# Optimization experiments

Hardware: AMD Instinct MI355X
Metric: run time of the kernel (lower is better)

Reference implementation:

```python
import jax, jax.numpy as jnp
import numpy as np

B, S, D = 8, 1024, 1024

def setup_inputs() -> dict:
    key = jax.random.key(0)
    ks = jax.random.split(key, 6)
    context = jax.random.normal(ks[0], (B, S, D), dtype=jnp.float32)
    eos_mask = jax.random.randint(ks[1], (B, S), 0, 2, dtype=jnp.int32)
    prior = jax.random.uniform(ks[2], (), dtype=jnp.float32)
    adj_mat = jax.random.randint(ks[3], (B, S, S), 0, 2, dtype=jnp.int32)
    Wk = jax.random.normal(ks[4], (D, D), dtype=jnp.float32) * 0.02
    Wq = jax.random.normal(ks[5], (D, D), dtype=jnp.float32) * 0.02
    bk = jnp.zeros((D,), jnp.float32)
    bq = jnp.zeros((D,), jnp.float32)
    ln_gamma = jnp.ones((D,), jnp.float32)
    ln_beta = jnp.zeros((D,), jnp.float32)
    return {"context": context, "eos_mask": eos_mask, "prior": prior,
            "adj_mat": adj_mat, "Wk": Wk, "bk": bk, "Wq": Wq, "bq": bq,
            "ln_gamma": ln_gamma, "ln_beta": ln_beta}

def reference(context, eos_mask, prior, adj_mat, Wk, bk, Wq, bq, ln_gamma, ln_beta):
    d_model = context.shape[-1]
    seq_len = context.shape[1]
    # LayerNorm (annotated-transformer style: unbiased std, eps added to std)
    mu = jnp.mean(context, axis=-1, keepdims=True)
    std = jnp.std(context, axis=-1, keepdims=True, ddof=1)
    x = ln_gamma * (context - mu) / (std + 1e-6) + ln_beta
    # projections (torch Linear: x @ W.T + b)
    key_p = x @ Wk.T + bk
    query = x @ Wq.T + bq
    scores = jnp.einsum('bqd,bkd->bqk', query, key_p) / (d_model / 2)
    scores = jnp.where(adj_mat == 0, -1e9, scores)
    neibor_attn = jax.nn.softmax(scores, axis=-1)
    neibor_attn = jnp.sqrt(neibor_attn * jnp.swapaxes(neibor_attn, -1, -2) + 1e-9)
    neibor_attn = prior + (1.0 - prior) * neibor_attn
    # constant structural matrices
    a = jnp.eye(seq_len, k=1, dtype=jnp.float32)          # superdiagonal
    b = jnp.eye(seq_len, dtype=jnp.float32)               # diagonal
    tri = jnp.triu(jnp.ones((seq_len, seq_len), jnp.float32))  # upper incl diag
    # t = (log(attn+eps) masked to superdiagonal) @ tri
    t = jnp.matmul(jnp.where(a == 0, 0.0, jnp.log(neibor_attn + 1e-9)), tri)
    g_attn = jnp.exp(jnp.matmul(tri, t))
    g_attn = jnp.where((tri - b) == 0, 0.0, g_attn)  # keep strict upper only
    g_attn = g_attn + jnp.swapaxes(g_attn, -1, -2) + jnp.where(b == 0, 1e-9, neibor_attn)
    return (g_attn, neibor_attn)
```

## Files before the change

kernel.cpp:

```cpp
#include <hip/hip_runtime.h>
#include <hip/hip_bf16.h>

#define S_LEN 1024
#define D_DIM 1024
#define N_BAT 8
#define BSS   (8ull*1024ull*1024ull)

using bf16x8 = __attribute__((ext_vector_type(8))) short;
using f32x4  = __attribute__((ext_vector_type(4))) float;

__device__ __forceinline__ short f2bf(float v) {
    __hip_bfloat16 h = __float2bfloat16(v);
    return *reinterpret_cast<short*>(&h);
}

__device__ __forceinline__ void gload_lds16(const void* g, void* l) {
    __builtin_amdgcn_global_load_lds(
        (const __attribute__((address_space(1))) void*)g,
        (__attribute__((address_space(3))) void*)l, 16, 0, 0);
}

template<int KITERS>
__device__ __forceinline__ void gemm_mainloop256(
    const short* __restrict__ A, const short* __restrict__ Bt,
    int brow, int bcol, int kstart,
    short* As, short* Bs, f32x4 acc[4][4])
{
    const int tid  = threadIdx.x;
    const int lane = tid & 63;
    const int w    = tid >> 6;
    const int wr   = w >> 1;
    const int wc   = w & 1;
    const int rsel = lane & 15;
    const int kb   = (lane >> 4) * 16;
    const int sw   = (rsel & 7) << 4;

    const int srow  = tid >> 3;
    const int scolb = ((tid & 7) * 16) ^ ((srow & 7) << 4);
    const int sdst  = tid * 16;

#pragma unroll
    for (int m = 0; m < 4; ++m)
#pragma unroll
        for (int n = 0; n < 4; ++n) acc[m][n] = 0.0f;

    auto stage = [&](int slot, int k0) {
        char* Ad = (char*)As + slot * 32768;
        char* Bd = (char*)Bs + slot * 16384;
#pragma unroll
        for (int c = 0; c < 4; ++c) {
            const int row = c * 64 + srow;
            gload_lds16((const char*)(A + (size_t)(brow + row) * 1024 + k0) + scolb,
                        Ad + c * 8192 + sdst);
        }
#pragma unroll
        for (int c = 0; c < 2; ++c) {
            const int row = c * 64 + srow;
            gload_lds16((const char*)(Bt + (size_t)(bcol + row) * 1024 + k0) + scolb,
                        Bd + c * 8192 + sdst);
        }
    };

    stage(0, kstart);
    if (KITERS > 1) stage(1, kstart + 64);

#pragma unroll
    for (int t = 0; t < KITERS; ++t) {
        if (t < KITERS - 1) asm volatile("s_waitcnt vmcnt(6)" ::: "memory");
        else                asm volatile("s_waitcnt vmcnt(0)" ::: "memory");
        __builtin_amdgcn_s_barrier();
        asm volatile("" ::: "memory");

        const char* Ac = (const char*)As + (t % 3) * 32768;
        const char* Bc = (const char*)Bs + (t % 3) * 16384;
        bf16x8 af[4][2], bfr[4][2];
#pragma unroll
        for (int m = 0; m < 4; ++m) {
            const int row = wr * 64 + m * 16 + rsel;
#pragma unroll
            for (int kk = 0; kk < 2; ++kk)
                af[m][kk] = *(const bf16x8*)&Ac[row * 128 + ((kk * 64 + kb) ^ sw)];
        }
#pragma unroll
        for (int n = 0; n < 4; ++n) {
            const int row = wc * 64 + n * 16 + rsel;
#pragma unroll
            for (int kk = 0; kk < 2; ++kk)
                bfr[n][kk] = *(const bf16x8*)&Bc[row * 128 + ((kk * 64 + kb) ^ sw)];
        }

        if (t + 2 < KITERS) stage((t + 2) % 3, kstart + (t + 2) * 64);

        __builtin_amdgcn_s_setprio(1);
#pragma unroll
        for (int kk = 0; kk < 2; ++kk)
#pragma unroll
            for (int m = 0; m < 4; ++m)
#pragma unroll
                for (int n = 0; n < 4; ++n)
                    acc[m][n] = __builtin_amdgcn_mfma_f32_16x16x32_bf16(
                        af[m][kk], bfr[n][kk], acc[m][n], 0, 0, 0);
        __builtin_amdgcn_s_setprio(0);
    }
}

__global__ __launch_bounds__(512) void gemm_bf16(
    const short* __restrict__ A, const short* __restrict__ Bt,
    short* __restrict__ C)
{
    __shared__ short As[3 * 16384];
    __shared__ short Bs[3 * 8192];
    const int flat = blockIdx.x + 32 * blockIdx.y;
    const int nid  = (flat & 7) * 32 + (flat >> 3);
    const int mx   = nid >> 3;
    const int ny   = nid & 7;
    const int brow = mx * 256, bcol = ny * 128;

    f32x4 acc[4][4];
    gemm_mainloop256<16>(A, Bt, brow, bcol, 0, As, Bs, acc);

    const int lane = threadIdx.x & 63;
    const int w    = threadIdx.x >> 6;
    const int wr   = w >> 1, wc = w & 1;
#pragma unroll
    for (int m = 0; m < 4; ++m)
#pragma unroll
        for (int n = 0; n < 4; ++n) {
            const int colg = bcol + wc * 64 + n * 16 + (lane & 15);
#pragma unroll
            for (int r = 0; r < 4; ++r) {
                const int rowg = brow + wr * 64 + m * 16 + ((lane >> 4) * 4 + r);
                C[(size_t)rowg * 1024 + colg] = f2bf(acc[m][n][r]);
            }
        }
}

__global__ __launch_bounds__(512) void gemm_scores(
    const short* __restrict__ Tm, const short* __restrict__ Xm,
    const float* __restrict__ p, const float* __restrict__ r2,
    const float* __restrict__ c0p, const int* __restrict__ adj,
    float* __restrict__ Sc)
{
    __shared__ short As[3 * 16384];
    __shared__ short Bs[3 * 8192];
    const int flat = blockIdx.x + 4 * blockIdx.y + 32 * blockIdx.z;
    const int nid  = (flat & 7) * 32 + (flat >> 3);
    const int b    = nid >> 5;
    const int rem  = nid & 31;
    const int mx   = rem & 3;
    const int ny   = rem >> 2;
    const short* A  = Tm + (size_t)b * 1024 * 1024;
    const short* Bt = Xm + (size_t)b * 1024 * 1024;
    const float* pb = p  + (size_t)b * 1024;
    const float* rb = r2 + (size_t)b * 1024;
    const int*   ab = adj + (size_t)b * 1024 * 1024;
    float* C = Sc + (size_t)b * 1024 * 1024;
    const int brow = mx * 256, bcol = ny * 128;

    f32x4 acc[4][4];
    gemm_mainloop256<16>(A, Bt, brow, bcol, 0, As, Bs, acc);

    const int lane = threadIdx.x & 63;
    const int w    = threadIdx.x >> 6;
    const int wr   = w >> 1, wc = w & 1;
    const float c0v = c0p[0];
#pragma unroll
    for (int m = 0; m < 4; ++m)
#pragma unroll
        for (int n = 0; n < 4; ++n) {
            const int colg = bcol + wc * 64 + n * 16 + (lane & 15);
            const float radd = rb[colg] + c0v;
#pragma unroll
            for (int r = 0; r < 4; ++r) {
                const int rowg = brow + wr * 64 + m * 16 + ((lane >> 4) * 4 + r);
                const size_t idx = (size_t)rowg * 1024 + colg;
                const float val = (acc[m][n][r] + pb[rowg] + radd) * 0.001953125f;
                C[idx] = ab[idx] ? val : -1e9f;
            }
        }
}

__global__ __launch_bounds__(512) void gemm_splitk(
    const short* __restrict__ A, const short* __restrict__ Bt,
    float* __restrict__ P)
{
    __shared__ short As[3 * 16384];
    __shared__ short Bs[3 * 8192];
    const int brow = blockIdx.x * 256, bcol = blockIdx.y * 128;
    const int z = blockIdx.z;

    f32x4 acc[4][4];
    gemm_mainloop256<4>(A, Bt, brow, bcol, z * 256, As, Bs, acc);

    float* Pz = P + (size_t)z * 1024 * 1024;
    const int lane = threadIdx.x & 63;
    const int w    = threadIdx.x >> 6;
    const int wr   = w >> 1, wc = w & 1;
#pragma unroll
    for (int m = 0; m < 4; ++m)
#pragma unroll
        for (int n = 0; n < 4; ++n) {
            const int colg = bcol + wc * 64 + n * 16 + (lane & 15);
#pragma unroll
            for (int r = 0; r < 4; ++r) {
                const int rowg = brow + wr * 64 + m * 16 + ((lane >> 4) * 4 + r);
                Pz[(size_t)rowg * 1024 + colg] = acc[m][n][r];
            }
        }
}

__global__ __launch_bounds__(256) void reduce_m2t(
    const float* __restrict__ P, short* __restrict__ M)
{
    const int idx = blockIdx.x * 256 + threadIdx.x;
    const float4* P4 = (const float4*)P;
    float4 s = P4[idx];
    const float4 s1 = P4[idx + 262144];
    const float4 s2 = P4[idx + 524288];
    const float4 s3 = P4[idx + 786432];
    s.x += s1.x + s2.x + s3.x;
    s.y += s1.y + s2.y + s3.y;
    s.z += s1.z + s2.z + s3.z;
    s.w += s1.w + s2.w + s3.w;
    short4 o;
    o.x = f2bf(s.x); o.y = f2bf(s.y); o.z = f2bf(s.z); o.w = f2bf(s.w);
    ((short4*)M)[idx] = o;
}

__global__ __launch_bounds__(256) void bias_gemv1(
    const float* __restrict__ Wq, const float* __restrict__ Wk,
    const float* __restrict__ bk, const float* __restrict__ bq,
    float* __restrict__ pu, float* __restrict__ pv)
{
    __shared__ float su[8][128];
    __shared__ float sv[8][128];
    const int tx = threadIdx.x & 31;
    const int ty = threadIdx.x >> 5;
    const int colBase = blockIdx.x * 128;
    const int rowBase = blockIdx.y * 64;
    const int i = colBase + tx * 4;
    float4 au = {0,0,0,0}, av = {0,0,0,0};
#pragma unroll
    for (int jj = 0; jj < 8; ++jj) {
        const int j = rowBase + ty + jj * 8;
        const float bkv = bk[j], bqv = bq[j];
        const float4 wq = *(const float4*)&Wq[(size_t)j * 1024 + i];
        const float4 wk = *(const float4*)&Wk[(size_t)j * 1024 + i];
        au.x += wq.x * bkv; au.y += wq.y * bkv; au.z += wq.z * bkv; au.w += wq.w * bkv;
        av.x += wk.x * bqv; av.y += wk.y * bqv; av.z += wk.z * bqv; av.w += wk.w * bqv;
    }
    ((float4*)su[ty])[tx] = au;
    ((float4*)sv[ty])[tx] = av;
    __syncthreads();
    if (ty == 0) {
        float4 s1 = ((float4*)su[0])[tx];
        float4 s2 = ((float4*)sv[0])[tx];
#pragma unroll
        for (int k = 1; k < 8; ++k) {
            const float4 t1 = ((float4*)su[k])[tx];
            const float4 t2 = ((float4*)sv[k])[tx];
            s1.x += t1.x; s1.y += t1.y; s1.z += t1.z; s1.w += t1.w;
            s2.x += t2.x; s2.y += t2.y; s2.z += t2.z; s2.w += t2.w;
        }
        ((float4*)&pu[(size_t)blockIdx.y * 1024 + colBase])[tx] = s1;
        ((float4*)&pv[(size_t)blockIdx.y * 1024 + colBase])[tx] = s2;
    }
}

__global__ __launch_bounds__(256) void bias_gemv2(
    const float* __restrict__ pu, const float* __restrict__ pv,
    const float* __restrict__ bk, const float* __restrict__ bq,
    float* __restrict__ u, float* __restrict__ v, float* __restrict__ c0)
{
    __shared__ float sh[4];
    const int i = blockIdx.x * 256 + threadIdx.x;
    float su = 0.0f, sv = 0.0f;
#pragma unroll
    for (int k = 0; k < 16; ++k) {
        su += pu[k * 1024 + i];
        sv += pv[k * 1024 + i];
    }
    u[i] = su;
    v[i] = sv;
    if (blockIdx.x == 0) {
        const int t = threadIdx.x;
        const float4 a = ((const float4*)bq)[t];
        const float4 b = ((const float4*)bk)[t];
        float s = a.x*b.x + a.y*b.y + a.z*b.z + a.w*b.w;
        for (int off = 32; off > 0; off >>= 1) s += __shfl_down(s, off);
        const int lane = t & 63, w = t >> 6;
        if (lane == 0) sh[w] = s;
        __syncthreads();
        if (t == 0) c0[0] = sh[0] + sh[1] + sh[2] + sh[3];
    }
}

__global__ __launch_bounds__(256) void ln_kernel(
    const float* __restrict__ X, const float* __restrict__ gamma,
    const float* __restrict__ beta, const float* __restrict__ u,
    const float* __restrict__ v2, short* __restrict__ Y,
    float* __restrict__ p, float* __restrict__ r2)
{
    __shared__ float sh[16];
    const size_t row = blockIdx.x;
    const int t = threadIdx.x;
    float4 v = ((const float4*)(X + row * 1024))[t];
    float s  = v.x + v.y + v.z + v.w;
    float ss = v.x*v.x + v.y*v.y + v.z*v.z + v.w*v.w;
    for (int off = 32; off > 0; off >>= 1) {
        s  += __shfl_down(s, off);
        ss += __shfl_down(ss, off);
    }
    const int lane = t & 63, w = t >> 6;
    if (lane == 0) { sh[w] = s; sh[4 + w] = ss; }
    __syncthreads();
    if (t == 0) {
        float S  = sh[0] + sh[1] + sh[2] + sh[3];
        float SS = sh[4] + sh[5] + sh[6] + sh[7];
        float mu = S * (1.0f / 1024.0f);
        float var = fmaxf((SS - S * mu) * (1.0f / 1023.0f), 0.0f);
        sh[0] = mu;
        sh[1] = 1.0f / (sqrtf(var) + 1e-6f);
    }
    __syncthreads();
    const float mu = sh[0], inv = sh[1];
    float4 g  = ((const float4*)gamma)[t];
    float4 be = ((const float4*)beta)[t];
    float y0 = g.x * (v.x - mu) * inv + be.x;
    float y1 = g.y * (v.y - mu) * inv + be.y;
    float y2 = g.z * (v.z - mu) * inv + be.z;
    float y3 = g.w * (v.w - mu) * inv + be.w;
    short4 o;
    o.x = f2bf(y0); o.y = f2bf(y1); o.z = f2bf(y2); o.w = f2bf(y3);
    ((short4*)(Y + row * 1024))[t] = o;
    float4 uu = ((const float4*)u)[t];
    float4 vv = ((const float4*)v2)[t];
    float dp = y0*uu.x + y1*uu.y + y2*uu.z + y3*uu.w;
    float dr = y0*vv.x + y1*vv.y + y2*vv.z + y3*vv.w;
    for (int off = 32; off > 0; off >>= 1) {
        dp += __shfl_down(dp, off);
        dr += __shfl_down(dr, off);
    }
    if (lane == 0) { sh[8 + w] = dp; sh[12 + w] = dr; }
    __syncthreads();
    if (t == 0) {
        p[row]  = sh[8] + sh[9] + sh[10] + sh[11];
        r2[row] = sh[12] + sh[13] + sh[14] + sh[15];
    }
}

__global__ __launch_bounds__(256) void cvt_t_kernel(
    const float* __restrict__ Wq, const float* __restrict__ Wk,
    short* __restrict__ wqt, short* __restrict__ wkt)
{
    __shared__ float T[32][33];
    const float* src = blockIdx.z ? Wk : Wq;
    short* dst = blockIdx.z ? wkt : wqt;
    const int bi = blockIdx.x * 32, bj = blockIdx.y * 32;
    const int c = threadIdx.x & 31, r0 = threadIdx.x >> 5;
#pragma unroll
    for (int rr = 0; rr < 4; ++rr) {
        const int r = r0 + rr * 8;
        T[r][c] = src[(size_t)(bi + r) * 1024 + bj + c];
    }
    __syncthreads();
#pragma unroll
    for (int rr = 0; rr < 4; ++rr) {
        const int r = r0 + rr * 8;
        dst[(size_t)(bj + r) * 1024 + bi + c] = f2bf(T[c][r]);
    }
}

__global__ __launch_bounds__(256) void rowstat_kernel(
    const float* __restrict__ Sc, float2* __restrict__ stats)
{
    __shared__ float sh[4];
    const size_t row = blockIdx.x;
    const int t = threadIdx.x;
    const float4 sv = ((const float4*)(Sc + row * 1024))[t];
    float m = fmaxf(fmaxf(sv.x, sv.y), fmaxf(sv.z, sv.w));
    for (int off = 32; off > 0; off >>= 1) m = fmaxf(m, __shfl_down(m, off));
    const int lane = t & 63, w = t >> 6;
    if (lane == 0) sh[w] = m;
    __syncthreads();
    const float M = fmaxf(fmaxf(sh[0], sh[1]), fmaxf(sh[2], sh[3]));
    __syncthreads();
    float s = expf(sv.x - M) + expf(sv.y - M) + expf(sv.z - M) + expf(sv.w - M);
    for (int off = 32; off > 0; off >>= 1) s += __shfl_down(s, off);
    if (lane == 0) sh[w] = s;
    __syncthreads();
    if (t == 0) {
        const float Sm = sh[0] + sh[1] + sh[2] + sh[3];
        stats[row] = make_float2(M, 1.0f / Sm);
    }
}

__global__ __launch_bounds__(1024) void cum2_kernel(
    const float* __restrict__ Sc, const float2* __restrict__ stats,
    const float* __restrict__ prior_p, double* __restrict__ cum)
{
    __shared__ double sh[1024];
    const int b = blockIdx.x;
    const int t = threadIdx.x;
    const float prior = *prior_p;
    const float om = 1.0f - prior;
    const float* sc = Sc + (size_t)b * 1024 * 1024;
    const float2* st = stats + (size_t)b * 1024;
    double v = 0.0;
    if (t >= 1) {
        const int k = t - 1;
        const float2 s1 = st[k], s2 = st[k + 1];
        const float a1 = expf(sc[(size_t)k * 1024 + (k + 1)] - s1.x) * s1.y;
        const float a2 = expf(sc[(size_t)(k + 1) * 1024 + k] - s2.x) * s2.y;
        const float na = prior + om * sqrtf(a1 * a2 + 1e-9f);
        v = (double)logf(na + 1e-9f);
    }
    sh[t] = v;
    __syncthreads();
#pragma unroll
    for (int off = 1; off < 1024; off <<= 1) {
        const double add = (t >= off) ? sh[t - off] : 0.0;
        __syncthreads();
        sh[t] += add;
        __syncthreads();
    }
    cum[b * 1024 + t] = sh[t];
}

__global__ __launch_bounds__(256) void na_g2_kernel(
    float* __restrict__ Sc, const float2* __restrict__ stats,
    const float* __restrict__ prior_p, const double* __restrict__ cum,
    float* __restrict__ NA)
{
    const int flat = blockIdx.x + 1024 * blockIdx.y;
    const int nid  = (flat & 7) * 1024 + (flat >> 3);
    const int b    = nid >> 10;
    const int tidx = nid & 1023;
    const int ti = tidx >> 5, tj = tidx & 31;
    if (tj < ti) return;
    const float prior = *prior_p;
    const float om = 1.0f - prior;
    float* sc = Sc + (size_t)b * 1024 * 1024;
    float* na = NA + (size_t)b * 1024 * 1024;
    const float2* st = stats + (size_t)b * 1024;
    const double* cb = cum + (size_t)b * 1024;
    __shared__ float T1[32][33];
    __shared__ float T2[32][33];
    const int c = threadIdx.x & 31, r0 = threadIdx.x >> 5;
#pragma unroll
    for (int rr = 0; rr < 4; ++rr) {
        const int r = r0 + rr * 8;
        const int R1 = ti * 32 + r, R2 = tj * 32 + r;
        const float2 s1 = st[R1], s2 = st[R2];
        T1[r][c] = expf(sc[(size_t)R1 * 1024 + tj * 32 + c] - s1.x) * s1.y;
        T2[r][c] = expf(sc[(size_t)R2 * 1024 + ti * 32 + c] - s2.x) * s2.y;
    }
    __syncthreads();
#pragma unroll
    for (int rr = 0; rr < 4; ++rr) {
        const int r = r0 + rr * 8;
        const int R1 = ti * 32 + r, C1 = tj * 32 + c;
        const float na1 = prior + om * sqrtf(T1[r][c] * T2[c][r] + 1e-9f);
        na[(size_t)R1 * 1024 + C1] = na1;
        float g1;
        if (R1 == C1) g1 = na1;
        else {
            const int lo = min(R1, C1), hi = max(R1, C1);
            g1 = expf((float)(cb[hi] - cb[lo])) + 1e-9f;
        }
        sc[(size_t)R1 * 1024 + C1] = g1;
        const int R2 = tj * 32 + r, C2 = ti * 32 + c;
        const float na2 = prior + om * sqrtf(T2[r][c] * T1[c][r] + 1e-9f);
        na[(size_t)R2 * 1024 + C2] = na2;
        float g2;
        if (R2 == C2) g2 = na2;
        else {
            const int lo = min(R2, C2), hi = max(R2, C2);
            g2 = expf((float)(cb[hi] - cb[lo])) + 1e-9f;
        }
        sc[(size_t)R2 * 1024 + C2] = g2;
    }
}

extern "C" void kernel_launch(void* const* d_in, const int* in_sizes, int n_in,
                              void* d_out, int out_size, void* d_ws, size_t ws_size,
                              hipStream_t stream)
{
    const float* context = (const float*)d_in[0];
    const float* prior   = (const float*)d_in[2];
    const int*   adj     = (const int*)d_in[3];
    const float* Wk      = (const float*)d_in[4];
    const float* bk      = (const float*)d_in[5];
    const float* Wq      = (const float*)d_in[6];
    const float* bq      = (const float*)d_in[7];
    const float* gamma   = (const float*)d_in[8];
    const float* beta    = (const float*)d_in[9];

    float* out   = (float*)d_out;
    float* gout  = out;
    float* naout = out + BSS;

    char* ws = (char*)d_ws;
    short*  xb    = (short*)(ws);
    short*  wqt   = (short*)(ws + (16ull << 20));
    short*  wkt   = (short*)(ws + (18ull << 20));
    short*  m2t   = (short*)(ws + (20ull << 20));
    short*  tb    = (short*)(ws + (22ull << 20));
    float*  m2par = (float*)tb;
    double* cumd  = (double*)(ws + (38ull << 20));
    float*  uvec  = (float*)(ws + (38ull << 20) + (1ull << 16));
    float*  vvec  = uvec + 1024;
    float*  c0    = vvec + 1024;
    float*  pvec  = c0 + 64;
    float*  rvec  = pvec + 8192;
    float*  pu    = rvec + 8192;
    float*  pv    = pu + 16384;
    float2* statv = (float2*)(pv + 16384);

    bias_gemv1<<<dim3(8, 16), 256, 0, stream>>>(Wq, Wk, bk, bq, pu, pv);
    bias_gemv2<<<4, 256, 0, stream>>>(pu, pv, bk, bq, uvec, vvec, c0);
    ln_kernel<<<8192, 256, 0, stream>>>(context, gamma, beta, uvec, vvec,
                                        xb, pvec, rvec);
    cvt_t_kernel<<<dim3(32, 32, 2), 256, 0, stream>>>(Wq, Wk, wqt, wkt);
    gemm_splitk<<<dim3(4, 8, 4), 512, 0, stream>>>(wkt, wqt, m2par);
    reduce_m2t<<<1024, 256, 0, stream>>>(m2par, m2t);
    gemm_bf16<<<dim3(32, 8), 512, 0, stream>>>(xb, m2t, tb);
    gemm_scores<<<dim3(4, 8, 8), 512, 0, stream>>>(tb, xb, pvec, rvec, c0,
                                                   adj, gout);
    rowstat_kernel<<<8192, 256, 0, stream>>>(gout, statv);
    cum2_kernel<<<8, 1024, 0, stream>>>(gout, statv, prior, cumd);
    na_g2_kernel<<<dim3(1024, 8), 256, 0, stream>>>(gout, statv, prior, cumd,
                                                    naout);
}
```

Measured before the change: 123.2 us.

## Switch GEMMs to 256x256 tiles with 8-phase double-buffered pipelined mainloop

Replaces the 256x128 triple-buffered GEMM mainloop with a 256x256 tile, double-buffered, 4-phase-per-k-tile schedule. Global-to-LDS loads for the next tile are interleaved between MFMA quadrants, and barriers separate the phases. Each wave now computes 128x64 outputs with 8x4 accumulators, which raises reuse per LDS read. Grids are halved to match the larger tiles. The risks are fewer blocks (128 per GEMM on a large GPU), which can underfill CUs, and higher register pressure from the 32 accumulators.

```diff
diff --git a/kernel.cpp b/kernel.cpp
--- a/kernel.cpp
+++ b/kernel.cpp
@@ -20,133 +20,169 @@
         (__attribute__((address_space(3))) void*)l, 16, 0, 0);
 }
 
-template<int KITERS>
-__device__ __forceinline__ void gemm_mainloop256(
+#define RD_A(dst, bufb, MH)                                                  \
+    {                                                                        \
+        const char* _b = (const char*)As + (bufb);                           \
+        _Pragma("unroll")                                                    \
+        for (int _m = 0; _m < 4; ++_m) {                                     \
+            const int _row = wr * 128 + ((MH) * 4 + _m) * 16 + rsel;         \
+            const int _sw  = (_row & 7) << 4;                                \
+            _Pragma("unroll")                                                \
+            for (int _kk = 0; _kk < 2; ++_kk)                                \
+                dst[_m * 2 + _kk] = *(const bf16x8*)&_b[_row * 128 +         \
+                                        ((_kk * 64 + kb) ^ _sw)];            \
+        }                                                                    \
+    }
+
+#define RD_B(dst, bufb, NH)                                                  \
+    {                                                                        \
+        const char* _b = (const char*)Bs + (bufb);                           \
+        _Pragma("unroll")                                                    \
+        for (int _n = 0; _n < 2; ++_n) {                                     \
+            const int _row = wc * 64 + ((NH) * 2 + _n) * 16 + rsel;          \
+            const int _sw  = (_row & 7) << 4;                                \
+            _Pragma("unroll")                                                \
+            for (int _kk = 0; _kk < 2; ++_kk)                                \
+                dst[_n * 2 + _kk] = *(const bf16x8*)&_b[_row * 128 +         \
+                                        ((_kk * 64 + kb) ^ _sw)];            \
+        }                                                                    \
+    }
+
+#define MMA_Q(av, bv, MH, NH)                                                \
+    __builtin_amdgcn_s_setprio(1);                                           \
+    _Pragma("unroll")                                                        \
+    for (int _kk = 0; _kk < 2; ++_kk)                                        \
+        _Pragma("unroll")                                                    \
+        for (int _m = 0; _m < 4; ++_m)                                       \
+            _Pragma("unroll")                                                \
+            for (int _n = 0; _n < 2; ++_n)                                   \
+                acc[(MH) * 4 + _m][(NH) * 2 + _n] =                          \
+                    __builtin_amdgcn_mfma_f32_16x16x32_bf16(                 \
+                        av[_m * 2 + _kk], bv[_n * 2 + _kk],                  \
+                        acc[(MH) * 4 + _m][(NH) * 2 + _n], 0, 0, 0);         \
+    __builtin_amdgcn_s_setprio(0);
+
+#define PHASE_END()                                                          \
+    __builtin_amdgcn_s_barrier();                                            \
+    __builtin_amdgcn_sched_barrier(0);
+
+template<int KTILES>
+__device__ __forceinline__ void gemm_ml_8ph(
     const short* __restrict__ A, const short* __restrict__ Bt,
     int brow, int bcol, int kstart,
-    short* As, short* Bs, f32x4 acc[4][4])
+    short* As, short* Bs, f32x4 acc[8][4])
 {
     const int tid  = threadIdx.x;
     const int lane = tid & 63;
     const int w    = tid >> 6;
-    const int wr   = w >> 1;
-    const int wc   = w & 1;
+    const int wr   = w >> 2;
+    const int wc   = w & 3;
     const int rsel = lane & 15;
     const int kb   = (lane >> 4) * 16;
-    const int sw   = (rsel & 7) << 4;
-
-    const int srow  = tid >> 3;
-    const int scolb = ((tid & 7) * 16) ^ ((srow & 7) << 4);
-    const int sdst  = tid * 16;
-
-#pragma unroll
-    for (int m = 0; m < 4; ++m)
+
+    const int f0 = tid;
+    const int f1 = 512 + tid;
+    const int r0 = f0 >> 3, cb0 = ((f0 & 7) * 16) ^ ((r0 & 7) << 4);
+    const int r1 = f1 >> 3, cb1 = ((f1 & 7) * 16) ^ ((r1 & 7) << 4);
+
+#pragma unroll
+    for (int m = 0; m < 8; ++m)
 #pragma unroll
         for (int n = 0; n < 4; ++n) acc[m][n] = 0.0f;
 
-    auto stage = [&](int slot, int k0) {
-        char* Ad = (char*)As + slot * 32768;
-        char* Bd = (char*)Bs + slot * 16384;
-#pragma unroll
-        for (int c = 0; c < 4; ++c) {
-            const int row = c * 64 + srow;
-            gload_lds16((const char*)(A + (size_t)(brow + row) * 1024 + k0) + scolb,
-                        Ad + c * 8192 + sdst);
-        }
-#pragma unroll
-        for (int c = 0; c < 2; ++c) {
-            const int row = c * 64 + srow;
-            gload_lds16((const char*)(Bt + (size_t)(bcol + row) * 1024 + k0) + scolb,
-                        Bd + c * 8192 + sdst);
-        }
+    auto stageA = [&](int buf, int h, int k0) {
+        char* d = (char*)As + buf * 32768 + h * 16384;
+        gload_lds16((const char*)(A + (size_t)(brow + h * 128 + r0) * 1024 + k0) + cb0,
+                    d + f0 * 16);
+        gload_lds16((const char*)(A + (size_t)(brow + h * 128 + r1) * 1024 + k0) + cb1,
+                    d + f1 * 16);
     };
-
-    stage(0, kstart);
-    if (KITERS > 1) stage(1, kstart + 64);
-
-#pragma unroll
-    for (int t = 0; t < KITERS; ++t) {
-        if (t < KITERS - 1) asm volatile("s_waitcnt vmcnt(6)" ::: "memory");
-        else                asm volatile("s_waitcnt vmcnt(0)" ::: "memory");
+    auto stageB = [&](int buf, int h, int k0) {
+        char* d = (char*)Bs + buf * 32768 + h * 16384;
+        gload_lds16((const char*)(Bt + (size_t)(bcol + h * 128 + r0) * 1024 + k0) + cb0,
+                    d + f0 * 16);
+        gload_lds16((const char*)(Bt + (size_t)(bcol + h * 128 + r1) * 1024 + k0) + cb1,
+                    d + f1 * 16);
+    };
+
+    stageA(0, 0, kstart); stageA(0, 1, kstart);
+    stageB(0, 0, kstart); stageB(0, 1, kstart);
+
+    bf16x8 a[8], b0[4], b1[4];
+    for (int t = 0; t < KTILES; ++t) {
+        const int cur = t & 1, nxt = cur ^ 1;
+        const int curb = cur * 32768;
+        const int kn = kstart + (t + 1) * 64;
+        const bool pre = (t + 1 < KTILES);
+        if (pre) {
+            stageA(nxt, 0, kn);
+            asm volatile("s_waitcnt vmcnt(2)" ::: "memory");
+        } else {
+            asm volatile("s_waitcnt vmcnt(0)" ::: "memory");
+        }
         __builtin_amdgcn_s_barrier();
-        asm volatile("" ::: "memory");
-
-        const char* Ac = (const char*)As + (t % 3) * 32768;
-        const char* Bc = (const char*)Bs + (t % 3) * 16384;
-        bf16x8 af[4][2], bfr[4][2];
-#pragma unroll
-        for (int m = 0; m < 4; ++m) {
-            const int row = wr * 64 + m * 16 + rsel;
-#pragma unroll
-            for (int kk = 0; kk < 2; ++kk)
-                af[m][kk] = *(const bf16x8*)&Ac[row * 128 + ((kk * 64 + kb) ^ sw)];
-        }
-#pragma unroll
-        for (int n = 0; n < 4; ++n) {
-            const int row = wc * 64 + n * 16 + rsel;
-#pragma unroll
-            for (int kk = 0; kk < 2; ++kk)
-                bfr[n][kk] = *(const bf16x8*)&Bc[row * 128 + ((kk * 64 + kb) ^ sw)];
-        }
-
-        if (t + 2 < KITERS) stage((t + 2) % 3, kstart + (t + 2) * 64);
-
-        __builtin_amdgcn_s_setprio(1);
-#pragma unroll
-        for (int kk = 0; kk < 2; ++kk)
-#pragma unroll
-            for (int m = 0; m < 4; ++m)
-#pragma unroll
-                for (int n = 0; n < 4; ++n)
-                    acc[m][n] = __builtin_amdgcn_mfma_f32_16x16x32_bf16(
-                        af[m][kk], bfr[n][kk], acc[m][n], 0, 0, 0);
-        __builtin_amdgcn_s_setprio(0);
-    }
-}
-
-__global__ __launch_bounds__(512) void gemm_bf16(
+        __builtin_amdgcn_sched_barrier(0);
+        RD_A(a, curb, 0);
+        RD_B(b0, curb, 0);
+        MMA_Q(a, b0, 0, 0);
+        PHASE_END();
+        if (pre) stageA(nxt, 1, kn);
+        RD_B(b1, curb, 1);
+        MMA_Q(a, b1, 0, 1);
+        PHASE_END();
+        if (pre) stageB(nxt, 0, kn);
+        RD_A(a, curb, 1);
+        MMA_Q(a, b1, 1, 1);
+        PHASE_END();
+        if (pre) stageB(nxt, 1, kn);
+        MMA_Q(a, b0, 1, 0);
+        PHASE_END();
+    }
+}
+
+__global__ __launch_bounds__(512, 2) void gemm_bf16(
     const short* __restrict__ A, const short* __restrict__ Bt,
     short* __restrict__ C)
 {
-    __shared__ short As[3 * 16384];
-    __shared__ short Bs[3 * 8192];
+    __shared__ short As[2 * 16384];
+    __shared__ short Bs[2 * 16384];
     const int flat = blockIdx.x + 32 * blockIdx.y;
-    const int nid  = (flat & 7) * 32 + (flat >> 3);
-    const int mx   = nid >> 3;
-    const int ny   = nid & 7;
-    const int brow = mx * 256, bcol = ny * 128;
-
-    f32x4 acc[4][4];
-    gemm_mainloop256<16>(A, Bt, brow, bcol, 0, As, Bs, acc);
+    const int nid  = (flat & 7) * 16 + (flat >> 3);
+    const int mx   = nid >> 2;
+    const int ny   = nid & 3;
+    const int brow = mx * 256, bcol = ny * 256;
+
+    f32x4 acc[8][4];
+    gemm_ml_8ph<16>(A, Bt, brow, bcol, 0, As, Bs, acc);
 
     const int lane = threadIdx.x & 63;
     const int w    = threadIdx.x >> 6;
-    const int wr   = w >> 1, wc = w & 1;
-#pragma unroll
-    for (int m = 0; m < 4; ++m)
-#pragma unroll
-        for (int n = 0; n < 4; ++n) {
-            const int colg = bcol + wc * 64 + n * 16 + (lane & 15);
+    const int wr   = w >> 2, wc = w & 3;
+#pragma unroll
+    for (int mm = 0; mm < 8; ++mm)
+#pragma unroll
+        for (int nn = 0; nn < 4; ++nn) {
+            const int colg = bcol + wc * 64 + nn * 16 + (lane & 15);
 #pragma unroll
             for (int r = 0; r < 4; ++r) {
-                const int rowg = brow + wr * 64 + m * 16 + ((lane >> 4) * 4 + r);
-                C[(size_t)rowg * 1024 + colg] = f2bf(acc[m][n][r]);
+                const int rowg = brow + wr * 128 + mm * 16 + ((lane >> 4) * 4 + r);
+                C[(size_t)rowg * 1024 + colg] = f2bf(acc[mm][nn][r]);
             }
         }
 }
 
-__global__ __launch_bounds__(512) void gemm_scores(
+__global__ __launch_bounds__(512, 2) void gemm_scores(
     const short* __restrict__ Tm, const short* __restrict__ Xm,
     const float* __restrict__ p, const float* __restrict__ r2,
     const float* __restrict__ c0p, const int* __restrict__ adj,
     float* __restrict__ Sc)
 {
-    __shared__ short As[3 * 16384];
-    __shared__ short Bs[3 * 8192];
-    const int flat = blockIdx.x + 4 * blockIdx.y + 32 * blockIdx.z;
-    const int nid  = (flat & 7) * 32 + (flat >> 3);
-    const int b    = nid >> 5;
-    const int rem  = nid & 31;
+    __shared__ short As[2 * 16384];
+    __shared__ short Bs[2 * 16384];
+    const int flat = blockIdx.x + 4 * blockIdx.y + 16 * blockIdx.z;
+    const int nid  = (flat & 7) * 16 + (flat >> 3);
+    const int b    = nid >> 4;
+    const int rem  = nid & 15;
     const int mx   = rem & 3;
     const int ny   = rem >> 2;
     const short* A  = Tm + (size_t)b * 1024 * 1024;
@@ -155,56 +191,56 @@
     const float* rb = r2 + (size_t)b * 1024;
     const int*   ab = adj + (size_t)b * 1024 * 1024;
     float* C = Sc + (size_t)b * 1024 * 1024;
-    const int brow = mx * 256, bcol = ny * 128;
-
-    f32x4 acc[4][4];
-    gemm_mainloop256<16>(A, Bt, brow, bcol, 0, As, Bs, acc);
+    const int brow = mx * 256, bcol = ny * 256;
+
+    f32x4 acc[8][4];
+    gemm_ml_8ph<16>(A, Bt, brow, bcol, 0, As, Bs, acc);
 
     const int lane = threadIdx.x & 63;
     const int w    = threadIdx.x >> 6;
-    const int wr   = w >> 1, wc = w & 1;
+    const int wr   = w >> 2, wc = w & 3;
     const float c0v = c0p[0];
 #pragma unroll
-    for (int m = 0; m < 4; ++m)
-#pragma unroll
-        for (int n = 0; n < 4; ++n) {
-            const int colg = bcol + wc * 64 + n * 16 + (lane & 15);
+    for (int mm = 0; mm < 8; ++mm)
+#pragma unroll
+        for (int nn = 0; nn < 4; ++nn) {
+            const int colg = bcol + wc * 64 + nn * 16 + (lane & 15);
             const float radd = rb[colg] + c0v;
 #pragma unroll
             for (int r = 0; r < 4; ++r) {
-                const int rowg = brow + wr * 64 + m * 16 + ((lane >> 4) * 4 + r);
+                const int rowg = brow + wr * 128 + mm * 16 + ((lane >> 4) * 4 + r);
                 const size_t idx = (size_t)rowg * 1024 + colg;
-                const float val = (acc[m][n][r] + pb[rowg] + radd) * 0.001953125f;
+                const float val = (acc[mm][nn][r] + pb[rowg] + radd) * 0.001953125f;
                 C[idx] = ab[idx] ? val : -1e9f;
             }
         }
 }
 
-__global__ __launch_bounds__(512) void gemm_splitk(
+__global__ __launch_bounds__(512, 2) void gemm_splitk(
     const short* __restrict__ A, const short* __restrict__ Bt,
     float* __restrict__ P)
 {
-    __shared__ short As[3 * 16384];
-    __shared__ short Bs[3 * 8192];
-    const int brow = blockIdx.x * 256, bcol = blockIdx.y * 128;
+    __shared__ short As[2 * 16384];
+    __shared__ short Bs[2 * 16384];
+    const int brow = blockIdx.x * 256, bcol = blockIdx.y * 256;
     const int z = blockIdx.z;
 
-    f32x4 acc[4][4];
-    gemm_mainloop256<4>(A, Bt, brow, bcol, z * 256, As, Bs, acc);
+    f32x4 acc[8][4];
+    gemm_ml_8ph<4>(A, Bt, brow, bcol, z * 256, As, Bs, acc);
 
     float* Pz = P + (size_t)z * 1024 * 1024;
     const int lane = threadIdx.x & 63;
     const int w    = threadIdx.x >> 6;
-    const int wr   = w >> 1, wc = w & 1;
-#pragma unroll
-    for (int m = 0; m < 4; ++m)
-#pragma unroll
-        for (int n = 0; n < 4; ++n) {
-            const int colg = bcol + wc * 64 + n * 16 + (lane & 15);
+    const int wr   = w >> 2, wc = w & 3;
+#pragma unroll
+    for (int mm = 0; mm < 8; ++mm)
+#pragma unroll
+        for (int nn = 0; nn < 4; ++nn) {
+            const int colg = bcol + wc * 64 + nn * 16 + (lane & 15);
 #pragma unroll
             for (int r = 0; r < 4; ++r) {
-                const int rowg = brow + wr * 64 + m * 16 + ((lane >> 4) * 4 + r);
-                Pz[(size_t)rowg * 1024 + colg] = acc[m][n][r];
+                const int rowg = brow + wr * 128 + mm * 16 + ((lane >> 4) * 4 + r);
+                Pz[(size_t)rowg * 1024 + colg] = acc[mm][nn][r];
             }
         }
 }
@@ -522,10 +558,10 @@
     ln_kernel<<<8192, 256, 0, stream>>>(context, gamma, beta, uvec, vvec,
                                         xb, pvec, rvec);
     cvt_t_kernel<<<dim3(32, 32, 2), 256, 0, stream>>>(Wq, Wk, wqt, wkt);
-    gemm_splitk<<<dim3(4, 8, 4), 512, 0, stream>>>(wkt, wqt, m2par);
+    gemm_splitk<<<dim3(4, 4, 4), 512, 0, stream>>>(wkt, wqt, m2par);
     reduce_m2t<<<1024, 256, 0, stream>>>(m2par, m2t);
-    gemm_bf16<<<dim3(32, 8), 512, 0, stream>>>(xb, m2t, tb);
-    gemm_scores<<<dim3(4, 8, 8), 512, 0, stream>>>(tb, xb, pvec, rvec, c0,
+    gemm_bf16<<<dim3(32, 4), 512, 0, stream>>>(xb, m2t, tb);
+    gemm_scores<<<dim3(4, 4, 8), 512, 0, stream>>>(tb, xb, pvec, rvec, c0,
                                                    adj, gout);
     rowstat_kernel<<<8192, 256, 0, stream>>>(gout, statv);
     cum2_kernel<<<8, 1024, 0, stream>>>(gout, statv, prior, cumd);
```

New measurement: 163.7 us. 32.9% more time.

## Double-buffer GEMM register fragments to overlap LDS reads with MFMA

Applied to the files above, without the earlier changes.

The bf16 GEMM mainloop now keeps two sets of register fragments. Fragments for the next K-stage are read from LDS while the MFMAs for the current stage run, instead of reading and then computing in strict sequence. The barrier and vmcnt waits move earlier, and an explicit lgkmcnt(0) wait before each barrier keeps the triple-buffered LDS slots safe from overwrite. This hides LDS latency behind tensor-core work, at the cost of roughly 64 extra VGPRs per lane for the second fragment set.

```diff
diff --git a/kernel.cpp b/kernel.cpp
--- a/kernel.cpp
+++ b/kernel.cpp
@@ -19,6 +19,40 @@
         (const __attribute__((address_space(1))) void*)g,
         (__attribute__((address_space(3))) void*)l, 16, 0, 0);
 }
+
+#define RDFRAG(slot, AF, BF)                                                  \
+    {                                                                         \
+        const char* _Ac = (const char*)As + (slot) * 32768;                   \
+        const char* _Bc = (const char*)Bs + (slot) * 16384;                   \
+        _Pragma("unroll")                                                     \
+        for (int _m = 0; _m < 4; ++_m) {                                      \
+            const int _row = wr * 64 + _m * 16 + rsel;                        \
+            _Pragma("unroll")                                                 \
+            for (int _kk = 0; _kk < 2; ++_kk)                                 \
+                AF[_m][_kk] = *(const bf16x8*)&_Ac[_row * 128 +               \
+                                                  ((_kk * 64 + kb) ^ sw)];    \
+        }                                                                     \
+        _Pragma("unroll")                                                     \
+        for (int _n = 0; _n < 4; ++_n) {                                      \
+            const int _row = wc * 64 + _n * 16 + rsel;                        \
+            _Pragma("unroll")                                                 \
+            for (int _kk = 0; _kk < 2; ++_kk)                                 \
+                BF[_n][_kk] = *(const bf16x8*)&_Bc[_row * 128 +               \
+                                                  ((_kk * 64 + kb) ^ sw)];    \
+        }                                                                     \
+    }
+
+#define MMA_ALL(AF, BF)                                                       \
+    __builtin_amdgcn_s_setprio(1);                                            \
+    _Pragma("unroll")                                                         \
+    for (int _kk = 0; _kk < 2; ++_kk)                                         \
+        _Pragma("unroll")                                                     \
+        for (int _m = 0; _m < 4; ++_m)                                        \
+            _Pragma("unroll")                                                  \
+            for (int _n = 0; _n < 4; ++_n)                                    \
+                acc[_m][_n] = __builtin_amdgcn_mfma_f32_16x16x32_bf16(        \
+                    AF[_m][_kk], BF[_n][_kk], acc[_m][_n], 0, 0, 0);          \
+    __builtin_amdgcn_s_setprio(0);
 
 template<int KITERS>
 __device__ __forceinline__ void gemm_mainloop256(
@@ -62,45 +96,32 @@
     };
 
     stage(0, kstart);
-    if (KITERS > 1) stage(1, kstart + 64);
+    if (KITERS > 1) {
+        stage(1, kstart + 64);
+        asm volatile("s_waitcnt vmcnt(6)" ::: "memory");
+    } else {
+        asm volatile("s_waitcnt vmcnt(0)" ::: "memory");
+    }
+    __builtin_amdgcn_s_barrier();
+    asm volatile("" ::: "memory");
+
+    bf16x8 af0[4][2], bf0[4][2], af1[4][2], bf1[4][2];
+    RDFRAG(0, af0, bf0);
 
 #pragma unroll
     for (int t = 0; t < KITERS; ++t) {
-        if (t < KITERS - 1) asm volatile("s_waitcnt vmcnt(6)" ::: "memory");
-        else                asm volatile("s_waitcnt vmcnt(0)" ::: "memory");
-        __builtin_amdgcn_s_barrier();
-        asm volatile("" ::: "memory");
-
-        const char* Ac = (const char*)As + (t % 3) * 32768;
-        const char* Bc = (const char*)Bs + (t % 3) * 16384;
-        bf16x8 af[4][2], bfr[4][2];
-#pragma unroll
-        for (int m = 0; m < 4; ++m) {
-            const int row = wr * 64 + m * 16 + rsel;
-#pragma unroll
-            for (int kk = 0; kk < 2; ++kk)
-                af[m][kk] = *(const bf16x8*)&Ac[row * 128 + ((kk * 64 + kb) ^ sw)];
-        }
-#pragma unroll
-        for (int n = 0; n < 4; ++n) {
-            const int row = wc * 64 + n * 16 + rsel;
-#pragma unroll
-            for (int kk = 0; kk < 2; ++kk)
-                bfr[n][kk] = *(const bf16x8*)&Bc[row * 128 + ((kk * 64 + kb) ^ sw)];
-        }
-
         if (t + 2 < KITERS) stage((t + 2) % 3, kstart + (t + 2) * 64);
-
-        __builtin_amdgcn_s_setprio(1);
-#pragma unroll
-        for (int kk = 0; kk < 2; ++kk)
-#pragma unroll
-            for (int m = 0; m < 4; ++m)
-#pragma unroll
-                for (int n = 0; n < 4; ++n)
-                    acc[m][n] = __builtin_amdgcn_mfma_f32_16x16x32_bf16(
-                        af[m][kk], bfr[n][kk], acc[m][n], 0, 0, 0);
-        __builtin_amdgcn_s_setprio(0);
+        if (t + 2 < KITERS)      asm volatile("s_waitcnt vmcnt(6)" ::: "memory");
+        else if (t + 1 < KITERS) asm volatile("s_waitcnt vmcnt(0)" ::: "memory");
+        if (t + 1 < KITERS) {
+            asm volatile("s_waitcnt lgkmcnt(0)" ::: "memory");
+            __builtin_amdgcn_s_barrier();
+            asm volatile("" ::: "memory");
+            if ((t & 1) == 0) { RDFRAG((t + 1) % 3, af1, bf1); }
+            else              { RDFRAG((t + 1) % 3, af0, bf0); }
+        }
+        if ((t & 1) == 0) { MMA_ALL(af0, bf0); }
+        else              { MMA_ALL(af1, bf1); }
     }
 }
 
```

Result: no change. 120.8 us (median of 2 runs) (-1.9%).
